# Kernel tuning notes

Measured on AMD Instinct MI355X. Metric: run time of the kernel, lower is better.

## Reference

```python
import jax, jax.numpy as jnp
import numpy as np

B, T, DM, DQ, DA, F, K = 128, 1024, 512, 1024, 128, 32, 31


def setup_inputs() -> dict:
    key = jax.random.key(0)
    ks = jax.random.split(key, 9)
    state = jax.random.uniform(ks[1], (B, T), dtype=jnp.float32)
    state = state / jnp.sum(state, axis=-1, keepdims=True)  # alignment-like
    return {
        "query": jax.random.normal(ks[0], (B, DQ), dtype=jnp.float32),
        "state": state,
        "prev_max_alignments": jax.random.randint(ks[2], (B,), 0, T, dtype=jnp.int32),
        "memory": jax.random.normal(ks[3], (B, T, DM), dtype=jnp.float32),
        "Wq": jax.random.normal(ks[4], (DQ, DA), dtype=jnp.float32) * 0.02,
        "Wmem": jax.random.normal(ks[5], (DM, DA), dtype=jnp.float32) * 0.02,
        "conv_k": jax.random.normal(ks[6], (K, 1, F), dtype=jnp.float32) * 0.02,
        "Wloc": jax.random.normal(ks[7], (F, DA), dtype=jnp.float32) * 0.02,
        "v_w": jax.random.normal(ks[8], (DA,), dtype=jnp.float32) * 0.02,
        "v_b": jnp.zeros((), dtype=jnp.float32),
    }


def reference(query, state, prev_max_alignments, memory, Wq, Wmem, conv_k, Wloc, v_w, v_b):
    # processed query: [B, 1, DA]
    pq = (query @ Wq)[:, None, :]
    # location features: Conv1D 'same', no bias, over cumulative alignments [B, T, 1]
    f = jax.lax.conv_general_dilated(
        state[:, :, None], conv_k,
        window_strides=(1,), padding="SAME",
        dimension_numbers=("NWC", "WIO", "NWC"),
    )  # [B, T, F]
    loc = f @ Wloc                      # [B, T, DA]
    keys = memory @ Wmem                # [B, T, DA]
    # additive tanh score -> [B, T]
    energy = jnp.tanh(keys + pq + loc) @ v_w + v_b
    alignments = jax.nn.softmax(energy, axis=-1)
    new_state = alignments + state      # is_cumulate=True
    # context: [B, DM]
    context = jnp.einsum("bt,btd->bd", alignments, memory)
    return context, alignments, new_state
```

## Files before the change

kernel.cpp:

```cpp
#include <hip/hip_runtime.h>
#include <math.h>

#define B  128
#define T  1024
#define DM 512
#define DQ 1024
#define DA 128
#define F  32
#define KW 31
#define TSEG 4

typedef short s16x8 __attribute__((ext_vector_type(8)));
typedef float f32x4 __attribute__((ext_vector_type(4)));
typedef unsigned int u32;
typedef u32 u32x4 __attribute__((ext_vector_type(4)));
typedef __attribute__((address_space(1))) const unsigned int gu32;
typedef __attribute__((address_space(3))) unsigned int lu32;

__device__ __forceinline__ unsigned short f2bf(float f) {
    u32 u = __builtin_bit_cast(u32, f);
    u32 r = u + 0x7FFFu + ((u >> 16) & 1u);
    return (unsigned short)(r >> 16);
}
__device__ __forceinline__ float bf2f(unsigned short h) {
    u32 u = ((u32)h) << 16;
    return __builtin_bit_cast(float, u);
}
__device__ __forceinline__ float fast_tanh(float x) {
    float ax = fabsf(x);
    float e = __expf(-2.0f * ax);
    float t = 1.0f - 2.0f * e / (1.0f + e);
    return copysignf(t, x);
}

__device__ __forceinline__ void trunc_split_pack(f32x4 a, f32x4 b, s16x8& hi, s16x8& lo) {
    u32x4 hw, lw;
    #pragma unroll
    for (int p = 0; p < 4; ++p) {
        float f0 = (p < 2) ? a[2 * p] : b[2 * p - 4];
        float f1 = (p < 2) ? a[2 * p + 1] : b[2 * p - 3];
        u32 u0 = __builtin_bit_cast(u32, f0);
        u32 u1 = __builtin_bit_cast(u32, f1);
        u32 t0 = u0 & 0xFFFF0000u;
        u32 t1 = u1 & 0xFFFF0000u;
        float l0 = f0 - __builtin_bit_cast(float, t0);
        float l1 = f1 - __builtin_bit_cast(float, t1);
        hw[p] = (u0 >> 16) | t1;
        lw[p] = (__builtin_bit_cast(u32, l0) >> 16) | (__builtin_bit_cast(u32, l1) & 0xFFFF0000u);
    }
    hi = __builtin_bit_cast(s16x8, hw);
    lo = __builtin_bit_cast(s16x8, lw);
}

__global__ __launch_bounds__(128) void prep_kernel(
        const float* __restrict__ query, const float* __restrict__ Wq,
        const float* __restrict__ Wmem, const float* __restrict__ conv_k,
        const float* __restrict__ Wloc,
        float* __restrict__ pqp, unsigned short* __restrict__ wsplit,
        unsigned short* __restrict__ CWt) {
    int a = threadIdx.x;
    int blk = blockIdx.x;
    if (blk < 4 * B) {
        int b = blk >> 2, q = blk & 3;
        const float* qp = query + b * DQ + q * 256;
        const float* wp = Wq + (size_t)(q * 256) * DA + a;
        float s = 0.f;
        #pragma unroll 4
        for (int i = 0; i < 256; ++i) s += qp[i] * wp[(size_t)i * DA];
        pqp[(q * B + b) * DA + a] = s;
    } else if (blk < 4 * B + DM) {
        int k = blk - 4 * B;
        unsigned short hi = f2bf(Wmem[k * DA + a]);
        int c = k >> 6;
        int es = (k & 63) ^ ((a & 7) << 3);
        wsplit[c * 8192 + a * 64 + es] = hi;
    } else {
        int k = blk - (4 * B + DM);
        float s = 0.f;
        if (k < KW) {
            #pragma unroll
            for (int f = 0; f < F; ++f) s += conv_k[k * F + f] * Wloc[f * DA + a];
        }
        CWt[a * 32 + k] = f2bf(s);
    }
}

__global__ __launch_bounds__(256, 4) void energy_mfma(
        const float* __restrict__ memory, const float* __restrict__ state,
        const float* __restrict__ pqp, const unsigned short* __restrict__ wsplit,
        const unsigned short* __restrict__ CWt, const float* __restrict__ v_w,
        const float* __restrict__ v_b, float* __restrict__ energy) {
    __shared__ unsigned short Wlds[8192];
    __shared__ unsigned short cwlds[4096];
    __shared__ float stl[160];
    __shared__ float pql[DA];
    __shared__ float vwl[DA];

    int tid = threadIdx.x;
    int w = tid >> 6, l = tid & 63, r = l & 15, g = l >> 4;
    int b  = blockIdx.x >> 3;
    int t0 = (blockIdx.x & 7) << 7;

    for (int i = tid; i < 160; i += 256) {
        int t = t0 - 15 + i;
        stl[i] = (i < 159 && t >= 0 && t < T) ? state[b * T + t] : 0.f;
    }
    if (tid < DA) {
        float s = 0.f;
        #pragma unroll
        for (int q = 0; q < 4; ++q) s += pqp[(q * B + b) * DA + tid];
        pql[tid] = s;
        vwl[tid] = v_w[tid];
    }

    #pragma unroll
    for (int rd = 0; rd < 2; ++rd)
        __builtin_amdgcn_global_load_lds((gu32*)(CWt + rd * 2048 + tid * 8),
                                         (lu32*)(cwlds + (w << 9) + rd * 2048), 16, 0, 0);

    f32x4 acc0[8], acc1[8];
    #pragma unroll
    for (int nt = 0; nt < 8; ++nt) {
        acc0[nt] = (f32x4){0.f, 0.f, 0.f, 0.f};
        acc1[nt] = (f32x4){0.f, 0.f, 0.f, 0.f};
    }

    const int swz8 = (r & 7) << 3;
    const size_t arow = ((size_t)(b * T + t0 + w * 32 + r)) * DM;

    for (int c = 0; c < 8; ++c) {
        __syncthreads();
        {
            const unsigned short* src = wsplit + (size_t)c * 8192 + tid * 8;
            #pragma unroll
            for (int rd = 0; rd < 4; ++rd)
                __builtin_amdgcn_global_load_lds((gu32*)(src + rd * 2048),
                                                 (lu32*)(Wlds + (w << 9) + rd * 2048),
                                                 16, 0, 0);
        }
        __syncthreads();

        const float* Ab = memory + arow + c * 64;
        #pragma unroll
        for (int kk = 0; kk < 2; ++kk) {
            const float* p0 = Ab + kk * 32 + g * 8;
            f32x4 f00 = *(const f32x4*)p0;
            f32x4 f01 = *(const f32x4*)(p0 + 4);
            const float* p1 = p0 + 16 * DM;
            f32x4 f10 = *(const f32x4*)p1;
            f32x4 f11 = *(const f32x4*)(p1 + 4);
            s16x8 Ah0, Al0, Ah1, Al1;
            trunc_split_pack(f00, f01, Ah0, Al0);
            trunc_split_pack(f10, f11, Ah1, Al1);
            int off = (kk * 32 + g * 8) ^ swz8;
            #pragma unroll
            for (int nt = 0; nt < 8; ++nt) {
                const unsigned short* bp = Wlds + (nt * 16 + r) * 64 + off;
                s16x8 Bh = *(const s16x8*)bp;
                acc0[nt] = __builtin_amdgcn_mfma_f32_16x16x32_bf16(Ah0, Bh, acc0[nt], 0, 0, 0);
                acc0[nt] = __builtin_amdgcn_mfma_f32_16x16x32_bf16(Al0, Bh, acc0[nt], 0, 0, 0);
                acc1[nt] = __builtin_amdgcn_mfma_f32_16x16x32_bf16(Ah1, Bh, acc1[nt], 0, 0, 0);
                acc1[nt] = __builtin_amdgcn_mfma_f32_16x16x32_bf16(Al1, Bh, acc1[nt], 0, 0, 0);
            }
        }
    }

    s16x8 st0, st1;
    {
        int base0 = w * 32 + r + g * 8;
        #pragma unroll
        for (int j = 0; j < 8; ++j) {
            st0[j] = (short)f2bf(stl[base0 + j]);
            st1[j] = (short)f2bf(stl[base0 + 16 + j]);
        }
    }
    #pragma unroll
    for (int nt = 0; nt < 8; ++nt) {
        const unsigned short* cp = cwlds + (nt * 16 + r) * 32 + g * 8;
        s16x8 cw = *(const s16x8*)cp;
        acc0[nt] = __builtin_amdgcn_mfma_f32_16x16x32_bf16(st0, cw, acc0[nt], 0, 0, 0);
        acc1[nt] = __builtin_amdgcn_mfma_f32_16x16x32_bf16(st1, cw, acc1[nt], 0, 0, 0);
    }

    float vb = *v_b;
    #pragma unroll
    for (int sub = 0; sub < 2; ++sub) {
        #pragma unroll
        for (int reg = 0; reg < 4; ++reg) {
            float p = 0.f;
            #pragma unroll
            for (int nt = 0; nt < 8; ++nt) {
                int col = nt * 16 + r;
                float v = (sub == 0) ? acc0[nt][reg] : acc1[nt][reg];
                p += fast_tanh(v + pql[col]) * vwl[col];
            }
            p += __shfl_xor(p, 1, 16);
            p += __shfl_xor(p, 2, 16);
            p += __shfl_xor(p, 4, 16);
            p += __shfl_xor(p, 8, 16);
            if (r == 0)
                energy[b * T + t0 + w * 32 + sub * 16 + g * 4 + reg] = p + vb;
        }
    }
}

__global__ __launch_bounds__(256) void softmax_context_kernel(
        const float* __restrict__ energy, const float* __restrict__ state,
        const float* __restrict__ memory,
        float* __restrict__ alignments, float* __restrict__ new_state,
        float* __restrict__ partial) {
    int b = blockIdx.x, seg = blockIdx.y, tid = threadIdx.x;
    __shared__ float rmax[4], rsum[4];
    __shared__ float al[T / TSEG];
    __shared__ f32x4 comb[128];

    f32x4 ev = ((const f32x4*)(energy + b * T))[tid];
    float m = fmaxf(fmaxf(ev[0], ev[1]), fmaxf(ev[2], ev[3]));
    #pragma unroll
    for (int off = 32; off > 0; off >>= 1) m = fmaxf(m, __shfl_xor(m, off, 64));
    if ((tid & 63) == 0) rmax[tid >> 6] = m;
    __syncthreads();
    m = fmaxf(fmaxf(rmax[0], rmax[1]), fmaxf(rmax[2], rmax[3]));
    f32x4 x;
    x[0] = __expf(ev[0] - m); x[1] = __expf(ev[1] - m);
    x[2] = __expf(ev[2] - m); x[3] = __expf(ev[3] - m);
    float s = x[0] + x[1] + x[2] + x[3];
    #pragma unroll
    for (int off = 32; off > 0; off >>= 1) s += __shfl_xor(s, off, 64);
    if ((tid & 63) == 0) rsum[tid >> 6] = s;
    __syncthreads();
    s = rsum[0] + rsum[1] + rsum[2] + rsum[3];
    float inv = 1.0f / s;
    f32x4 a4 = x * inv;
    if ((tid >> 6) == seg) {
        ((f32x4*)al)[tid & 63] = a4;
        ((f32x4*)(alignments + b * T))[tid] = a4;
        f32x4 st4 = ((const f32x4*)(state + b * T))[tid];
        ((f32x4*)(new_state + b * T))[tid] = a4 + st4;
    }
    __syncthreads();

    int half = tid >> 7;
    int dg = tid & 127;
    const float* memB = memory + ((size_t)b * T + seg * (T / TSEG)) * DM;
    f32x4 acc = (f32x4){0.f, 0.f, 0.f, 0.f};
    #pragma unroll 4
    for (int it = 0; it < 128; ++it) {
        int t = it * 2 + half;
        float a = al[t];
        f32x4 v = *(const f32x4*)(memB + (size_t)t * DM + dg * 4);
        acc += v * a;
    }
    if (half) comb[dg] = acc;
    __syncthreads();
    if (!half) {
        acc += comb[dg];
        ((f32x4*)(partial + ((size_t)seg * B + b) * DM))[dg] = acc;
    }
}

__global__ __launch_bounds__(256) void context_reduce_kernel(
        const float* __restrict__ partial, float* __restrict__ context) {
    int b = blockIdx.x;
    int tid = threadIdx.x;
    #pragma unroll
    for (int j = 0; j < 2; ++j) {
        int d = tid + j * 256;
        float s = 0.f;
        #pragma unroll
        for (int g = 0; g < TSEG; ++g) s += partial[((size_t)g * B + b) * DM + d];
        context[b * DM + d] = s;
    }
}

extern "C" void kernel_launch(void* const* d_in, const int* in_sizes, int n_in,
                              void* d_out, int out_size, void* d_ws, size_t ws_size,
                              hipStream_t stream) {
    const float* query  = (const float*)d_in[0];
    const float* state  = (const float*)d_in[1];
    const float* memory = (const float*)d_in[3];
    const float* Wq     = (const float*)d_in[4];
    const float* Wmem   = (const float*)d_in[5];
    const float* conv_k = (const float*)d_in[6];
    const float* Wloc   = (const float*)d_in[7];
    const float* v_w    = (const float*)d_in[8];
    const float* v_b    = (const float*)d_in[9];

    float* out        = (float*)d_out;
    float* context    = out;
    float* alignments = out + B * DM;
    float* new_state  = out + B * DM + B * T;

    char* ws = (char*)d_ws;
    float*          pqp     = (float*)ws;
    unsigned short* wsplit  = (unsigned short*)(ws + 262144);
    unsigned short* CWt     = (unsigned short*)(ws + 524288);
    float*          energy  = (float*)(ws + 532480);
    float*          partial = (float*)(ws + 1056768);

    prep_kernel<<<dim3(4 * B + DM + 32), 128, 0, stream>>>(query, Wq, Wmem, conv_k, Wloc, pqp, wsplit, CWt);
    energy_mfma<<<dim3(B * (T / 128)), 256, 0, stream>>>(memory, state, pqp, wsplit, CWt, v_w, v_b, energy);
    softmax_context_kernel<<<dim3(B, TSEG), 256, 0, stream>>>(energy, state, memory, alignments, new_state, partial);
    context_reduce_kernel<<<dim3(B), 256, 0, stream>>>(partial, context);
}
```

Baseline: 128.4 us.

## Load weight tiles directly from global and register-prefetch memory rows

```diff
diff --git a/kernel.cpp b/kernel.cpp
--- a/kernel.cpp
+++ b/kernel.cpp
@@ -14,8 +14,6 @@
 typedef float f32x4 __attribute__((ext_vector_type(4)));
 typedef unsigned int u32;
 typedef u32 u32x4 __attribute__((ext_vector_type(4)));
-typedef __attribute__((address_space(1))) const unsigned int gu32;
-typedef __attribute__((address_space(3))) unsigned int lu32;
 
 __device__ __forceinline__ unsigned short f2bf(float f) {
     u32 u = __builtin_bit_cast(u32, f);
@@ -72,8 +70,7 @@
         int k = blk - 4 * B;
         unsigned short hi = f2bf(Wmem[k * DA + a]);
         int c = k >> 6;
-        int es = (k & 63) ^ ((a & 7) << 3);
-        wsplit[c * 8192 + a * 64 + es] = hi;
+        wsplit[c * 8192 + a * 64 + (k & 63)] = hi;
     } else {
         int k = blk - (4 * B + DM);
         float s = 0.f;
@@ -85,13 +82,11 @@
     }
 }
 
-__global__ __launch_bounds__(256, 4) void energy_mfma(
+__global__ __launch_bounds__(256, 2) void energy_mfma(
         const float* __restrict__ memory, const float* __restrict__ state,
         const float* __restrict__ pqp, const unsigned short* __restrict__ wsplit,
         const unsigned short* __restrict__ CWt, const float* __restrict__ v_w,
         const float* __restrict__ v_b, float* __restrict__ energy) {
-    __shared__ unsigned short Wlds[8192];
-    __shared__ unsigned short cwlds[4096];
     __shared__ float stl[160];
     __shared__ float pql[DA];
     __shared__ float vwl[DA];
@@ -112,11 +107,7 @@
         pql[tid] = s;
         vwl[tid] = v_w[tid];
     }
-
-    #pragma unroll
-    for (int rd = 0; rd < 2; ++rd)
-        __builtin_amdgcn_global_load_lds((gu32*)(CWt + rd * 2048 + tid * 8),
-                                         (lu32*)(cwlds + (w << 9) + rd * 2048), 16, 0, 0);
+    __syncthreads();
 
     f32x4 acc0[8], acc1[8];
     #pragma unroll
@@ -125,44 +116,53 @@
         acc1[nt] = (f32x4){0.f, 0.f, 0.f, 0.f};
     }
 
-    const int swz8 = (r & 7) << 3;
     const size_t arow = ((size_t)(b * T + t0 + w * 32 + r)) * DM;
+    const float* Abase = memory + arow + g * 8;
+    const unsigned short* Bbase = wsplit + r * 64 + g * 8;
+
+    f32x4 rA[8], rAn[8];
+    {
+        const float* p = Abase;
+        #pragma unroll
+        for (int kk = 0; kk < 2; ++kk) {
+            rA[kk * 4 + 0] = *(const f32x4*)(p + kk * 32);
+            rA[kk * 4 + 1] = *(const f32x4*)(p + kk * 32 + 4);
+            rA[kk * 4 + 2] = *(const f32x4*)(p + kk * 32 + 16 * DM);
+            rA[kk * 4 + 3] = *(const f32x4*)(p + kk * 32 + 16 * DM + 4);
+        }
+    }
 
     for (int c = 0; c < 8; ++c) {
-        __syncthreads();
-        {
-            const unsigned short* src = wsplit + (size_t)c * 8192 + tid * 8;
-            #pragma unroll
-            for (int rd = 0; rd < 4; ++rd)
-                __builtin_amdgcn_global_load_lds((gu32*)(src + rd * 2048),
-                                                 (lu32*)(Wlds + (w << 9) + rd * 2048),
-                                                 16, 0, 0);
-        }
-        __syncthreads();
-
-        const float* Ab = memory + arow + c * 64;
+        if (c < 7) {
+            const float* p = Abase + (c + 1) * 64;
+            #pragma unroll
+            for (int kk = 0; kk < 2; ++kk) {
+                rAn[kk * 4 + 0] = *(const f32x4*)(p + kk * 32);
+                rAn[kk * 4 + 1] = *(const f32x4*)(p + kk * 32 + 4);
+                rAn[kk * 4 + 2] = *(const f32x4*)(p + kk * 32 + 16 * DM);
+                rAn[kk * 4 + 3] = *(const f32x4*)(p + kk * 32 + 16 * DM + 4);
+            }
+        }
+        const unsigned short* Bc = Bbase + c * 8192;
         #pragma unroll
         for (int kk = 0; kk < 2; ++kk) {
-            const float* p0 = Ab + kk * 32 + g * 8;
-            f32x4 f00 = *(const f32x4*)p0;
-            f32x4 f01 = *(const f32x4*)(p0 + 4);
-            const float* p1 = p0 + 16 * DM;
-            f32x4 f10 = *(const f32x4*)p1;
-            f32x4 f11 = *(const f32x4*)(p1 + 4);
             s16x8 Ah0, Al0, Ah1, Al1;
-            trunc_split_pack(f00, f01, Ah0, Al0);
-            trunc_split_pack(f10, f11, Ah1, Al1);
-            int off = (kk * 32 + g * 8) ^ swz8;
+            trunc_split_pack(rA[kk * 4 + 0], rA[kk * 4 + 1], Ah0, Al0);
+            trunc_split_pack(rA[kk * 4 + 2], rA[kk * 4 + 3], Ah1, Al1);
+            s16x8 Bv[8];
+            #pragma unroll
+            for (int nt = 0; nt < 8; ++nt)
+                Bv[nt] = *(const s16x8*)(Bc + nt * 1024 + kk * 32);
             #pragma unroll
             for (int nt = 0; nt < 8; ++nt) {
-                const unsigned short* bp = Wlds + (nt * 16 + r) * 64 + off;
-                s16x8 Bh = *(const s16x8*)bp;
-                acc0[nt] = __builtin_amdgcn_mfma_f32_16x16x32_bf16(Ah0, Bh, acc0[nt], 0, 0, 0);
-                acc0[nt] = __builtin_amdgcn_mfma_f32_16x16x32_bf16(Al0, Bh, acc0[nt], 0, 0, 0);
-                acc1[nt] = __builtin_amdgcn_mfma_f32_16x16x32_bf16(Ah1, Bh, acc1[nt], 0, 0, 0);
-                acc1[nt] = __builtin_amdgcn_mfma_f32_16x16x32_bf16(Al1, Bh, acc1[nt], 0, 0, 0);
+                acc0[nt] = __builtin_amdgcn_mfma_f32_16x16x32_bf16(Ah0, Bv[nt], acc0[nt], 0, 0, 0);
+                acc0[nt] = __builtin_amdgcn_mfma_f32_16x16x32_bf16(Al0, Bv[nt], acc0[nt], 0, 0, 0);
+                acc1[nt] = __builtin_amdgcn_mfma_f32_16x16x32_bf16(Ah1, Bv[nt], acc1[nt], 0, 0, 0);
+                acc1[nt] = __builtin_amdgcn_mfma_f32_16x16x32_bf16(Al1, Bv[nt], acc1[nt], 0, 0, 0);
             }
         }
+        #pragma unroll
+        for (int j = 0; j < 8; ++j) rA[j] = rAn[j];
     }
 
     s16x8 st0, st1;
@@ -176,8 +176,7 @@
     }
     #pragma unroll
     for (int nt = 0; nt < 8; ++nt) {
-        const unsigned short* cp = cwlds + (nt * 16 + r) * 32 + g * 8;
-        s16x8 cw = *(const s16x8*)cp;
+        s16x8 cw = *(const s16x8*)(CWt + (nt * 16 + r) * 32 + g * 8);
         acc0[nt] = __builtin_amdgcn_mfma_f32_16x16x32_bf16(st0, cw, acc0[nt], 0, 0, 0);
         acc1[nt] = __builtin_amdgcn_mfma_f32_16x16x32_bf16(st1, cw, acc1[nt], 0, 0, 0);
     }
```

New measurement: 171.4 us. 1.34x slower.

## Fuse online-softmax context partials into energy kernel, add finalize rescale kernel

Applied to the files above, without the earlier changes.

```diff
diff --git a/kernel.cpp b/kernel.cpp
--- a/kernel.cpp
+++ b/kernel.cpp
@@ -8,7 +8,6 @@
 #define DA 128
 #define F  32
 #define KW 31
-#define TSEG 4
 
 typedef short s16x8 __attribute__((ext_vector_type(8)));
 typedef float f32x4 __attribute__((ext_vector_type(4)));
@@ -89,17 +88,20 @@
         const float* __restrict__ memory, const float* __restrict__ state,
         const float* __restrict__ pqp, const unsigned short* __restrict__ wsplit,
         const unsigned short* __restrict__ CWt, const float* __restrict__ v_w,
-        const float* __restrict__ v_b, float* __restrict__ energy) {
+        const float* __restrict__ v_b, float* __restrict__ energy,
+        float* __restrict__ pctx, float2* __restrict__ ms) {
     __shared__ unsigned short Wlds[8192];
     __shared__ unsigned short cwlds[4096];
     __shared__ float stl[160];
     __shared__ float pql[DA];
     __shared__ float vwl[DA];
+    __shared__ float el[128];
 
     int tid = threadIdx.x;
     int w = tid >> 6, l = tid & 63, r = l & 15, g = l >> 4;
     int b  = blockIdx.x >> 3;
-    int t0 = (blockIdx.x & 7) << 7;
+    int tile = blockIdx.x & 7;
+    int t0 = tile << 7;
 
     for (int i = tid; i < 160; i += 256) {
         int t = t0 - 15 + i;
@@ -198,78 +200,75 @@
             p += __shfl_xor(p, 2, 16);
             p += __shfl_xor(p, 4, 16);
             p += __shfl_xor(p, 8, 16);
-            if (r == 0)
-                energy[b * T + t0 + w * 32 + sub * 16 + g * 4 + reg] = p + vb;
-        }
-    }
-}
-
-__global__ __launch_bounds__(256) void softmax_context_kernel(
+            if (r == 0) {
+                int tl = w * 32 + sub * 16 + g * 4 + reg;
+                energy[b * T + t0 + tl] = p + vb;
+                el[tl] = p + vb;
+            }
+        }
+    }
+    __syncthreads();
+
+    float m_w = -1e30f;
+    #pragma unroll
+    for (int t = 0; t < 32; ++t) m_w = fmaxf(m_w, el[w * 32 + t]);
+    float s_w = 0.f;
+    f32x4 c0 = (f32x4){0.f, 0.f, 0.f, 0.f};
+    f32x4 c1 = (f32x4){0.f, 0.f, 0.f, 0.f};
+    const float* mb = memory + ((size_t)(b * T + t0 + w * 32)) * DM + l * 8;
+    #pragma unroll 4
+    for (int t = 0; t < 32; ++t) {
+        float pw = __expf(el[w * 32 + t] - m_w);
+        s_w += pw;
+        f32x4 v0 = *(const f32x4*)(mb + (size_t)t * DM);
+        f32x4 v1 = *(const f32x4*)(mb + (size_t)t * DM + 4);
+        c0 += pw * v0;
+        c1 += pw * v1;
+    }
+    float* po = pctx + ((size_t)(tile * 4 + w) * B + b) * DM + l * 8;
+    *(f32x4*)po = c0;
+    *(f32x4*)(po + 4) = c1;
+    if (l == 0) ms[(tile * 4 + w) * B + b] = make_float2(m_w, s_w);
+}
+
+__global__ __launch_bounds__(256) void finalize_kernel(
         const float* __restrict__ energy, const float* __restrict__ state,
-        const float* __restrict__ memory,
+        const float2* __restrict__ ms, const float* __restrict__ pctx,
         float* __restrict__ alignments, float* __restrict__ new_state,
-        float* __restrict__ partial) {
-    int b = blockIdx.x, seg = blockIdx.y, tid = threadIdx.x;
-    __shared__ float rmax[4], rsum[4];
-    __shared__ float al[T / TSEG];
-    __shared__ f32x4 comb[128];
+        float* __restrict__ context) {
+    int b = blockIdx.x, tid = threadIdx.x;
+    float m = -1e30f;
+    #pragma unroll
+    for (int i = 0; i < 32; ++i) m = fmaxf(m, ms[i * B + b].x);
+    float sc[32];
+    float S = 0.f;
+    #pragma unroll
+    for (int i = 0; i < 32; ++i) {
+        float2 v = ms[i * B + b];
+        float e = __expf(v.x - m);
+        sc[i] = e;
+        S += e * v.y;
+    }
+    float invS = 1.0f / S;
 
     f32x4 ev = ((const f32x4*)(energy + b * T))[tid];
-    float m = fmaxf(fmaxf(ev[0], ev[1]), fmaxf(ev[2], ev[3]));
-    #pragma unroll
-    for (int off = 32; off > 0; off >>= 1) m = fmaxf(m, __shfl_xor(m, off, 64));
-    if ((tid & 63) == 0) rmax[tid >> 6] = m;
-    __syncthreads();
-    m = fmaxf(fmaxf(rmax[0], rmax[1]), fmaxf(rmax[2], rmax[3]));
-    f32x4 x;
-    x[0] = __expf(ev[0] - m); x[1] = __expf(ev[1] - m);
-    x[2] = __expf(ev[2] - m); x[3] = __expf(ev[3] - m);
-    float s = x[0] + x[1] + x[2] + x[3];
-    #pragma unroll
-    for (int off = 32; off > 0; off >>= 1) s += __shfl_xor(s, off, 64);
-    if ((tid & 63) == 0) rsum[tid >> 6] = s;
-    __syncthreads();
-    s = rsum[0] + rsum[1] + rsum[2] + rsum[3];
-    float inv = 1.0f / s;
-    f32x4 a4 = x * inv;
-    if ((tid >> 6) == seg) {
-        ((f32x4*)al)[tid & 63] = a4;
-        ((f32x4*)(alignments + b * T))[tid] = a4;
-        f32x4 st4 = ((const f32x4*)(state + b * T))[tid];
-        ((f32x4*)(new_state + b * T))[tid] = a4 + st4;
-    }
-    __syncthreads();
-
-    int half = tid >> 7;
-    int dg = tid & 127;
-    const float* memB = memory + ((size_t)b * T + seg * (T / TSEG)) * DM;
-    f32x4 acc = (f32x4){0.f, 0.f, 0.f, 0.f};
-    #pragma unroll 4
-    for (int it = 0; it < 128; ++it) {
-        int t = it * 2 + half;
-        float a = al[t];
-        f32x4 v = *(const f32x4*)(memB + (size_t)t * DM + dg * 4);
-        acc += v * a;
-    }
-    if (half) comb[dg] = acc;
-    __syncthreads();
-    if (!half) {
-        acc += comb[dg];
-        ((f32x4*)(partial + ((size_t)seg * B + b) * DM))[dg] = acc;
-    }
-}
-
-__global__ __launch_bounds__(256) void context_reduce_kernel(
-        const float* __restrict__ partial, float* __restrict__ context) {
-    int b = blockIdx.x;
-    int tid = threadIdx.x;
+    f32x4 a4;
+    a4[0] = __expf(ev[0] - m) * invS;
+    a4[1] = __expf(ev[1] - m) * invS;
+    a4[2] = __expf(ev[2] - m) * invS;
+    a4[3] = __expf(ev[3] - m) * invS;
+    ((f32x4*)(alignments + b * T))[tid] = a4;
+    f32x4 st4 = ((const f32x4*)(state + b * T))[tid];
+    ((f32x4*)(new_state + b * T))[tid] = a4 + st4;
+
     #pragma unroll
     for (int j = 0; j < 2; ++j) {
         int d = tid + j * 256;
-        float s = 0.f;
-        #pragma unroll
-        for (int g = 0; g < TSEG; ++g) s += partial[((size_t)g * B + b) * DM + d];
-        context[b * DM + d] = s;
+        float c = 0.f;
+        #pragma unroll 8
+        for (int i = 0; i < 32; ++i)
+            c += sc[i] * pctx[((size_t)i * B + b) * DM + d];
+        context[b * DM + d] = c * invS;
     }
 }
 
@@ -296,10 +295,10 @@
     unsigned short* wsplit  = (unsigned short*)(ws + 262144);
     unsigned short* CWt     = (unsigned short*)(ws + 524288);
     float*          energy  = (float*)(ws + 532480);
-    float*          partial = (float*)(ws + 1056768);
+    float*          pctx    = (float*)(ws + 1056768);
+    float2*         ms      = (float2*)(ws + 1056768 + 8388608);
 
     prep_kernel<<<dim3(4 * B + DM + 32), 128, 0, stream>>>(query, Wq, Wmem, conv_k, Wloc, pqp, wsplit, CWt);
-    energy_mfma<<<dim3(B * (T / 128)), 256, 0, stream>>>(memory, state, pqp, wsplit, CWt, v_w, v_b, energy);
-    softmax_context_kernel<<<dim3(B, TSEG), 256, 0, stream>>>(energy, state, memory, alignments, new_state, partial);
-    context_reduce_kernel<<<dim3(B), 256, 0, stream>>>(partial, context);
-}
+    energy_mfma<<<dim3(B * (T / 128)), 256, 0, stream>>>(memory, state, pqp, wsplit, CWt, v_w, v_b, energy, pctx, ms);
+    finalize_kernel<<<dim3(B), 256, 0, stream>>>(energy, state, ms, pctx, alignments, new_state, context);
+}
```

Measured after the change: 121.6 us. 5.2% less time.
